# Performance work log

Measured on AMD Instinct MI355X. Metric: run time of the kernel, lower is better.

The kernel has to match this reference:

```python
import jax, jax.numpy as jnp
import numpy as np

D_MODEL = 1024
NUM_HEADS = 16
HEAD_DIM = D_MODEL // NUM_HEADS


def setup_inputs() -> dict:
    key = jax.random.key(0)
    k1, k2, k3, k4, k5 = jax.random.split(key, 5)
    B, S, D = 2, 2048, D_MODEL
    x = jax.random.normal(k1, (B, S, D), dtype=jnp.float32)
    mask = jnp.zeros((S, S), dtype=jnp.float32)  # additive mask, broadcast over [H,B,S,S]
    # torch nn.Linear params: weight [out, in], bias [out]
    scale_qkv = 1.0 / np.sqrt(D)
    W_qkv = jax.random.uniform(k2, (3 * D, D), jnp.float32, -scale_qkv, scale_qkv)
    b_qkv = jax.random.uniform(k3, (3 * D,), jnp.float32, -scale_qkv, scale_qkv)
    W_out = jax.random.uniform(k4, (D, D), jnp.float32, -scale_qkv, scale_qkv)
    b_out = jax.random.uniform(k5, (D,), jnp.float32, -scale_qkv, scale_qkv)
    return {"x": x, "mask": mask, "W_qkv": W_qkv, "b_qkv": b_qkv, "W_out": W_out, "b_out": b_out}


def reference(x, mask, W_qkv, b_qkv, W_out, b_out):
    B, S, D = x.shape
    H, hd = NUM_HEADS, HEAD_DIM
    # qkv projection: Linear(d, 3d) -> reshape [B,S,H,3*hd] -> [B,H,S,3*hd] -> chunk
    qkv = jnp.einsum('bsd,ed->bse', x, W_qkv) + b_qkv          # [B,S,3D]
    qkv = qkv.reshape(B, S, H, 3 * hd).transpose(0, 2, 1, 3)   # [B,H,S,3*hd]
    q, k, v = jnp.split(qkv, 3, axis=-1)                       # each [B,H,S,hd]
    scaled = jnp.einsum('bhqd,bhkd->bhqk', q, k) / jnp.sqrt(jnp.float32(hd))
    scaled = scaled + mask                                      # [S,S] broadcasts like the permuted add
    attn = jax.nn.softmax(scaled, axis=-1)
    values = jnp.einsum('bhqk,bhkd->bhqd', attn, v)            # [B,H,S,hd]
    values = values.transpose(0, 2, 1, 3).reshape(B, S, H * hd)
    out = jnp.einsum('bsd,ed->bse', values, W_out) + b_out
    return out
```

## Files before the change

### kernel.cpp

```cpp
#include <hip/hip_runtime.h>

#define SEQ   2048
#define BATCH 2
#define NH    16
#define HD    64
#define DM    1024

typedef unsigned short u16;
typedef unsigned int   u32;
typedef __attribute__((ext_vector_type(8))) short bf8;
typedef __attribute__((ext_vector_type(4))) float f4;

__device__ inline u16 f2bf(float f) {
    u32 u = __builtin_bit_cast(u32, f);
    return (u16)((u + 0x7FFFu + ((u >> 16) & 1u)) >> 16);
}

__device__ inline f4 MFMA(bf8 a, bf8 b, f4 c) {
    return __builtin_amdgcn_mfma_f32_16x16x32_bf16(a, b, c, 0, 0, 0);
}

__device__ inline void gload16(const u16* g, u16* l) {
    __builtin_amdgcn_global_load_lds(
        (const __attribute__((address_space(1))) unsigned int*)(const void*)g,
        (__attribute__((address_space(3))) unsigned int*)(void*)l, 16, 0, 0);
}

#define N4_X  1048576
#define N4_WQ 786432
#define N4_WO 262144
__global__ __launch_bounds__(256) void cast_all(const float* __restrict__ x,
                                                const float* __restrict__ wq,
                                                const float* __restrict__ wo,
                                                u16* __restrict__ xb,
                                                u16* __restrict__ wqb,
                                                u16* __restrict__ wob) {
    const int i = blockIdx.x * 256 + threadIdx.x;
    const float* src;
    u16* dst;
    int j;
    if (i < N4_X)                { src = x;  dst = xb;  j = i; }
    else if (i < N4_X + N4_WQ)   { src = wq; dst = wqb; j = i - N4_X; }
    else                         { src = wo; dst = wob; j = i - N4_X - N4_WQ; }
    const float4 v = ((const float4*)src)[j];
    ushort4 o;
    o.x = f2bf(v.x); o.y = f2bf(v.y); o.z = f2bf(v.z); o.w = f2bf(v.w);
    ((ushort4*)dst)[j] = o;
}

template<int MODE>
__global__ __launch_bounds__(256) void gemm_bf16(const u16* __restrict__ A,
                                                 const u16* __restrict__ Bm,
                                                 const float* __restrict__ bias,
                                                 u16* __restrict__ q_o,
                                                 u16* __restrict__ k_o,
                                                 u16* __restrict__ v_o,
                                                 float* __restrict__ f_o) {
    __shared__ __align__(16) u16 Al[128 * 32];
    __shared__ __align__(16) u16 Bl[128 * 32];
    const int t  = threadIdx.x;
    const int l  = t & 63, w = t >> 6;
    const int n0 = blockIdx.x * 128, m0 = blockIdx.y * 128;
    const int wr = w >> 1, wc = w & 1;
    const int lr16 = l & 15, lg = l >> 4;

    const f4 zf = {0.f, 0.f, 0.f, 0.f};
    f4 acc[4][4];
#pragma unroll
    for (int m = 0; m < 4; ++m)
#pragma unroll
        for (int n = 0; n < 4; ++n) acc[m][n] = zf;

    const int rw = t >> 2;
    const int kc = t & 3;

    for (int k0 = 0; k0 < DM; k0 += 32) {
        __syncthreads();
        gload16(&A[(size_t)(m0 + rw) * DM + k0 + kc * 8],       &Al[rw * 32 + kc * 8]);
        gload16(&A[(size_t)(m0 + 64 + rw) * DM + k0 + kc * 8],  &Al[(64 + rw) * 32 + kc * 8]);
        gload16(&Bm[(size_t)(n0 + rw) * DM + k0 + kc * 8],      &Bl[rw * 32 + kc * 8]);
        gload16(&Bm[(size_t)(n0 + 64 + rw) * DM + k0 + kc * 8], &Bl[(64 + rw) * 32 + kc * 8]);
        __syncthreads();
        bf8 af[4], bfr[4];
#pragma unroll
        for (int m = 0; m < 4; ++m)
            af[m] = *(const bf8*)&Al[(wr * 64 + m * 16 + lr16) * 32 + lg * 8];
#pragma unroll
        for (int n = 0; n < 4; ++n)
            bfr[n] = *(const bf8*)&Bl[(wc * 64 + n * 16 + lr16) * 32 + lg * 8];
        __builtin_amdgcn_s_setprio(1);
#pragma unroll
        for (int m = 0; m < 4; ++m)
#pragma unroll
            for (int n = 0; n < 4; ++n)
                acc[m][n] = MFMA(af[m], bfr[n], acc[m][n]);
        __builtin_amdgcn_s_setprio(0);
    }

#pragma unroll
    for (int m = 0; m < 4; ++m)
#pragma unroll
        for (int n = 0; n < 4; ++n)
#pragma unroll
            for (int r = 0; r < 4; ++r) {
                const int M = m0 + wr * 64 + m * 16 + lg * 4 + r;
                const int N = n0 + wc * 64 + n * 16 + lr16;
                const float val = acc[m][n][r] + bias[N];
                if (MODE == 0) {
                    const int b = M >> 11, s = M & (SEQ - 1);
                    const int h = N / 192, f = N % 192;
                    const int seg = f >> 6, c = f & 63;
                    u16* dst = (seg == 0) ? q_o : ((seg == 1) ? k_o : v_o);
                    dst[(((size_t)(b * NH + h)) * SEQ + s) * HD + c] = f2bf(val);
                } else {
                    f_o[(size_t)M * DM + N] = val;
                }
            }
}

__global__ __launch_bounds__(256) void v_transpose(const u16* __restrict__ v,
                                                   u16* __restrict__ vt) {
    __shared__ u16 tl[64][65];
    const int t  = threadIdx.x;
    const int s0 = blockIdx.x * 64;
    const int bh = blockIdx.y;
    const u16* src = v + ((size_t)bh * SEQ + s0) * HD;
#pragma unroll
    for (int i = 0; i < 2; ++i) {
        const int c = i * 256 + t, s = c >> 3, cc = c & 7;
        const float4 d = *(const float4*)&src[s * HD + cc * 8];
        const u16* dp = (const u16*)&d;
#pragma unroll
        for (int j = 0; j < 8; ++j) tl[s][cc * 8 + j] = dp[j];
    }
    __syncthreads();
    u16* dst = vt + (size_t)bh * HD * SEQ + s0;
#pragma unroll
    for (int i = 0; i < 2; ++i) {
        const int c = i * 256 + t, dim = c >> 3, sc = c & 7;
        __align__(16) u16 tmp[8];
#pragma unroll
        for (int j = 0; j < 8; ++j) tmp[j] = tl[sc * 8 + j][dim];
        *(float4*)&dst[(size_t)dim * SEQ + sc * 8] = *(const float4*)tmp;
    }
}

#define KS 72
__global__ __launch_bounds__(256) void flash_attn(const u16* __restrict__ qg,
                                                  const u16* __restrict__ kg,
                                                  const u16* __restrict__ vtg,
                                                  const float* __restrict__ mask,
                                                  u16* __restrict__ og) {
    __shared__ __align__(16) u16 Kl[2][64 * KS];
    __shared__ __align__(16) u16 Vl[2][64 * KS];
    __shared__ __align__(16) u16 Pl[4 * 16 * KS];
    const int t = threadIdx.x, l = t & 63, w = t >> 6;
    const int lr16 = l & 15, lg = l >> 4;
    const int q0 = blockIdx.x * 64;
    const int h = blockIdx.y, b = blockIdx.z;
    const int bh = b * NH + h;
    const int qbase = q0 + w * 16;

    bf8 qf[2];
    {
        const u16* qp = qg + ((size_t)bh * SEQ + qbase + lr16) * HD + lg * 8;
        qf[0] = *(const bf8*)qp;
        qf[1] = *(const bf8*)(qp + 32);
    }

    const f4 zf = {0.f, 0.f, 0.f, 0.f};
    f4 Oa[4];
    float mr[4], lrow[4];
#pragma unroll
    for (int n = 0; n < 4; ++n) Oa[n] = zf;
#pragma unroll
    for (int r = 0; r < 4; ++r) { mr[r] = -1e30f; lrow[r] = 0.f; }

    const u16* Kb = kg + (size_t)bh * SEQ * HD;
    const u16* Vb = vtg + (size_t)bh * HD * SEQ;
    u16* Pw = &Pl[w * 16 * KS];

    float4 kvr[2], vvr[2];
    float mk[4][4], mkn[4][4];

    auto issue_kv = [&](int kv0) {
#pragma unroll
        for (int i = 0; i < 2; ++i) {
            const int c = i * 256 + t, a = c >> 3, cc = c & 7;
            kvr[i] = *(const float4*)&Kb[(size_t)(kv0 + a) * HD + cc * 8];
            vvr[i] = *(const float4*)&Vb[(size_t)a * SEQ + kv0 + cc * 8];
        }
    };
    auto write_kv = [&](int buf) {
#pragma unroll
        for (int i = 0; i < 2; ++i) {
            const int c = i * 256 + t, a = c >> 3, cc = c & 7;
            *(float4*)&Kl[buf][a * KS + cc * 8] = kvr[i];
            *(float4*)&Vl[buf][a * KS + cc * 8] = vvr[i];
        }
    };
    auto issue_mask = [&](float (&m)[4][4], int kv0) {
#pragma unroll
        for (int n = 0; n < 4; ++n)
#pragma unroll
            for (int r = 0; r < 4; ++r)
                m[n][r] = mask[(size_t)(q0 + w * 16 + lg * 4 + r) * SEQ + kv0 + n * 16 + lr16];
    };

    issue_kv(0);
    issue_mask(mk, 0);
    write_kv(0);
    issue_kv(64);
    issue_mask(mkn, 64);
    __syncthreads();

    for (int kt = 0; kt < 32; ++kt) {
        const int cur = kt & 1;
        f4 sc[4];
        __builtin_amdgcn_s_setprio(1);
#pragma unroll
        for (int n = 0; n < 4; ++n) {
            const bf8 k0 = *(const bf8*)&Kl[cur][(n * 16 + lr16) * KS + lg * 8];
            const bf8 k1 = *(const bf8*)&Kl[cur][(n * 16 + lr16) * KS + 32 + lg * 8];
            f4 s = zf;
            s = MFMA(qf[0], k0, s);
            s = MFMA(qf[1], k1, s);
            sc[n] = s;
        }
        __builtin_amdgcn_s_setprio(0);
#pragma unroll
        for (int n = 0; n < 4; ++n)
#pragma unroll
            for (int r = 0; r < 4; ++r)
                sc[n][r] = sc[n][r] * 0.125f + mk[n][r];
        float pmax[4];
#pragma unroll
        for (int r = 0; r < 4; ++r) {
            float mx = fmaxf(fmaxf(sc[0][r], sc[1][r]), fmaxf(sc[2][r], sc[3][r]));
#pragma unroll
            for (int d = 1; d < 16; d <<= 1) mx = fmaxf(mx, __shfl_xor(mx, d));
            pmax[r] = mx;
        }
        bool need = false;
#pragma unroll
        for (int r = 0; r < 4; ++r) need |= (pmax[r] > mr[r] + 8.f);
        if (__any(need)) {
#pragma unroll
            for (int r = 0; r < 4; ++r) {
                const float mn = fmaxf(mr[r], pmax[r]);
                const float al = __expf(mr[r] - mn);
                mr[r] = mn;
                lrow[r] *= al;
#pragma unroll
                for (int n = 0; n < 4; ++n) Oa[n][r] *= al;
            }
        }
        float rs[4] = {0.f, 0.f, 0.f, 0.f};
        u16 pb[4][4];
#pragma unroll
        for (int n = 0; n < 4; ++n)
#pragma unroll
            for (int r = 0; r < 4; ++r) {
                const float p = __expf(sc[n][r] - mr[r]);
                rs[r] += p;
                pb[n][r] = f2bf(p);
            }
#pragma unroll
        for (int r = 0; r < 4; ++r) {
            float s = rs[r];
#pragma unroll
            for (int d = 1; d < 16; d <<= 1) s += __shfl_xor(s, d);
            lrow[r] += s;
        }
#pragma unroll
        for (int n = 0; n < 4; ++n)
#pragma unroll
            for (int r = 0; r < 4; ++r)
                Pw[(lg * 4 + r) * KS + n * 16 + lr16] = pb[n][r];
        asm volatile("s_waitcnt lgkmcnt(0)" ::: "memory");
        const bf8 pf0 = *(const bf8*)&Pw[lr16 * KS + lg * 8];
        const bf8 pf1 = *(const bf8*)&Pw[lr16 * KS + 32 + lg * 8];
        __builtin_amdgcn_s_setprio(1);
#pragma unroll
        for (int n = 0; n < 4; ++n) {
            const bf8 v0 = *(const bf8*)&Vl[cur][(n * 16 + lr16) * KS + lg * 8];
            const bf8 v1 = *(const bf8*)&Vl[cur][(n * 16 + lr16) * KS + 32 + lg * 8];
            Oa[n] = MFMA(pf0, v0, Oa[n]);
            Oa[n] = MFMA(pf1, v1, Oa[n]);
        }
        __builtin_amdgcn_s_setprio(0);
        if (kt < 31) {
            write_kv(cur ^ 1);
#pragma unroll
            for (int n = 0; n < 4; ++n)
#pragma unroll
                for (int r = 0; r < 4; ++r) mk[n][r] = mkn[n][r];
            if (kt < 30) {
                issue_kv((kt + 2) * 64);
                issue_mask(mkn, (kt + 2) * 64);
            }
        }
        __syncthreads();
    }

    float inv[4];
#pragma unroll
    for (int r = 0; r < 4; ++r) inv[r] = 1.f / lrow[r];
    __syncthreads();
    u16* Ol = Pl;
#pragma unroll
    for (int n = 0; n < 4; ++n)
#pragma unroll
        for (int r = 0; r < 4; ++r)
            Ol[(w * 16 + lg * 4 + r) * KS + n * 16 + lr16] = f2bf(Oa[n][r] * inv[r]);
    __syncthreads();
    {
        const int row = t >> 2, c0 = (t & 3) * 16;
        const u16* src = &Ol[row * KS + c0];
        u16* dstp = og + ((size_t)(b * SEQ + q0 + row)) * DM + h * HD + c0;
        const float4 o0 = *(const float4*)src;
        const float4 o1 = *(const float4*)(src + 8);
        *(float4*)dstp = o0;
        *(float4*)(dstp + 8) = o1;
    }
}

extern "C" void kernel_launch(void* const* d_in, const int* in_sizes, int n_in,
                              void* d_out, int out_size, void* d_ws, size_t ws_size,
                              hipStream_t stream) {
    const float* x     = (const float*)d_in[0];
    const float* mask  = (const float*)d_in[1];
    const float* W_qkv = (const float*)d_in[2];
    const float* b_qkv = (const float*)d_in[3];
    const float* W_out = (const float*)d_in[4];
    const float* b_out = (const float*)d_in[5];
    float* out = (float*)d_out;

    const size_t NQ = (size_t)BATCH * NH * SEQ * HD;
    u16* ws  = (u16*)d_ws;
    u16* xb  = ws;
    u16* wqb = xb + (size_t)4096 * 1024;
    u16* wob = wqb + (size_t)3072 * 1024;
    u16* qb  = wob + (size_t)1024 * 1024;
    u16* kb  = qb + NQ;
    u16* vb  = kb + NQ;
    u16* vtb = vb + NQ;
    u16* ob  = vtb + NQ;

    cast_all<<<(N4_X + N4_WQ + N4_WO) / 256, 256, 0, stream>>>(x, W_qkv, W_out, xb, wqb, wob);
    gemm_bf16<0><<<dim3(24, 32), 256, 0, stream>>>(xb, wqb, b_qkv, qb, kb, vb, nullptr);
    v_transpose<<<dim3(32, 32), 256, 0, stream>>>(vb, vtb);
    flash_attn<<<dim3(SEQ / 64, NH, BATCH), 256, 0, stream>>>(qb, kb, vtb, mask, ob);
    gemm_bf16<1><<<dim3(8, 32), 256, 0, stream>>>(ob, wob, b_out, nullptr, nullptr, nullptr, out);
}
```

Baseline: 346.3 us.

## Process 32 query rows per wave in flash attention with exp2 softmax

```diff
diff --git a/kernel.cpp b/kernel.cpp
--- a/kernel.cpp
+++ b/kernel.cpp
@@ -1,4 +1,5 @@
 #include <hip/hip_runtime.h>
+#include <hip/hip_bf16.h>
 
 #define SEQ   2048
 #define BATCH 2
@@ -146,6 +147,7 @@
 }
 
 #define KS 72
+#define QW 32
 __global__ __launch_bounds__(256) void flash_attn(const u16* __restrict__ qg,
                                                   const u16* __restrict__ kg,
                                                   const u16* __restrict__ vtg,
@@ -153,35 +155,44 @@
                                                   u16* __restrict__ og) {
     __shared__ __align__(16) u16 Kl[2][64 * KS];
     __shared__ __align__(16) u16 Vl[2][64 * KS];
-    __shared__ __align__(16) u16 Pl[4 * 16 * KS];
+    __shared__ __align__(16) u16 Pl[4 * QW * KS];
     const int t = threadIdx.x, l = t & 63, w = t >> 6;
     const int lr16 = l & 15, lg = l >> 4;
-    const int q0 = blockIdx.x * 64;
-    const int h = blockIdx.y, b = blockIdx.z;
-    const int bh = b * NH + h;
-    const int qbase = q0 + w * 16;
-
-    bf8 qf[2];
-    {
-        const u16* qp = qg + ((size_t)bh * SEQ + qbase + lr16) * HD + lg * 8;
-        qf[0] = *(const bf8*)qp;
-        qf[1] = *(const bf8*)(qp + 32);
+    const int bx = blockIdx.x;
+    const int qt = bx >> 5, bh = bx & 31;
+    const int h = bh & 15, b = bh >> 4;
+    const int q0 = qt * 128;
+    const int qbase = q0 + w * QW;
+
+    const float C1 = 0.18033688011f;
+    const float L2E = 1.44269504089f;
+
+    bf8 qf[2][2];
+#pragma unroll
+    for (int m = 0; m < 2; ++m) {
+        const u16* qp = qg + ((size_t)bh * SEQ + qbase + m * 16 + lr16) * HD + lg * 8;
+        qf[m][0] = *(const bf8*)qp;
+        qf[m][1] = *(const bf8*)(qp + 32);
     }
 
     const f4 zf = {0.f, 0.f, 0.f, 0.f};
-    f4 Oa[4];
-    float mr[4], lrow[4];
-#pragma unroll
-    for (int n = 0; n < 4; ++n) Oa[n] = zf;
-#pragma unroll
-    for (int r = 0; r < 4; ++r) { mr[r] = -1e30f; lrow[r] = 0.f; }
+    f4 Oa[2][4];
+    float mr2[2][4], lp[2][4];
+#pragma unroll
+    for (int m = 0; m < 2; ++m)
+#pragma unroll
+        for (int n = 0; n < 4; ++n) Oa[m][n] = zf;
+#pragma unroll
+    for (int m = 0; m < 2; ++m)
+#pragma unroll
+        for (int r = 0; r < 4; ++r) { mr2[m][r] = -1e30f; lp[m][r] = 0.f; }
 
     const u16* Kb = kg + (size_t)bh * SEQ * HD;
     const u16* Vb = vtg + (size_t)bh * HD * SEQ;
-    u16* Pw = &Pl[w * 16 * KS];
+    u16* Pw = &Pl[w * QW * KS];
 
     float4 kvr[2], vvr[2];
-    float mk[4][4], mkn[4][4];
+    float mk2[2][4][4], mkn2[2][4][4];
 
     auto issue_kv = [&](int kv0) {
 #pragma unroll
@@ -199,129 +210,147 @@
             *(float4*)&Vl[buf][a * KS + cc * 8] = vvr[i];
         }
     };
-    auto issue_mask = [&](float (&m)[4][4], int kv0) {
-#pragma unroll
-        for (int n = 0; n < 4; ++n)
-#pragma unroll
-            for (int r = 0; r < 4; ++r)
-                m[n][r] = mask[(size_t)(q0 + w * 16 + lg * 4 + r) * SEQ + kv0 + n * 16 + lr16];
+    auto issue_mask = [&](float (&mm)[2][4][4], int kv0) {
+#pragma unroll
+        for (int m = 0; m < 2; ++m)
+#pragma unroll
+            for (int n = 0; n < 4; ++n)
+#pragma unroll
+                for (int r = 0; r < 4; ++r)
+                    mm[m][n][r] = mask[(size_t)(qbase + m * 16 + lg * 4 + r) * SEQ
+                                       + kv0 + n * 16 + lr16] * L2E;
     };
 
     issue_kv(0);
-    issue_mask(mk, 0);
+    issue_mask(mk2, 0);
     write_kv(0);
     issue_kv(64);
-    issue_mask(mkn, 64);
+    issue_mask(mkn2, 64);
     __syncthreads();
 
     for (int kt = 0; kt < 32; ++kt) {
         const int cur = kt & 1;
-        f4 sc[4];
+        f4 sc[2][4];
         __builtin_amdgcn_s_setprio(1);
 #pragma unroll
         for (int n = 0; n < 4; ++n) {
             const bf8 k0 = *(const bf8*)&Kl[cur][(n * 16 + lr16) * KS + lg * 8];
             const bf8 k1 = *(const bf8*)&Kl[cur][(n * 16 + lr16) * KS + 32 + lg * 8];
-            f4 s = zf;
-            s = MFMA(qf[0], k0, s);
-            s = MFMA(qf[1], k1, s);
-            sc[n] = s;
+#pragma unroll
+            for (int m = 0; m < 2; ++m)
+                sc[m][n] = MFMA(qf[m][1], k1, MFMA(qf[m][0], k0, zf));
         }
         __builtin_amdgcn_s_setprio(0);
 #pragma unroll
-        for (int n = 0; n < 4; ++n)
-#pragma unroll
-            for (int r = 0; r < 4; ++r)
-                sc[n][r] = sc[n][r] * 0.125f + mk[n][r];
-        float pmax[4];
-#pragma unroll
-        for (int r = 0; r < 4; ++r) {
-            float mx = fmaxf(fmaxf(sc[0][r], sc[1][r]), fmaxf(sc[2][r], sc[3][r]));
-#pragma unroll
-            for (int d = 1; d < 16; d <<= 1) mx = fmaxf(mx, __shfl_xor(mx, d));
-            pmax[r] = mx;
-        }
+        for (int m = 0; m < 2; ++m)
+#pragma unroll
+            for (int n = 0; n < 4; ++n)
+#pragma unroll
+                for (int r = 0; r < 4; ++r)
+                    sc[m][n][r] = fmaf(sc[m][n][r], C1, mk2[m][n][r]);
+        float lmax[2][4];
         bool need = false;
 #pragma unroll
-        for (int r = 0; r < 4; ++r) need |= (pmax[r] > mr[r] + 8.f);
+        for (int m = 0; m < 2; ++m)
+#pragma unroll
+            for (int r = 0; r < 4; ++r) {
+                lmax[m][r] = fmaxf(fmaxf(sc[m][0][r], sc[m][1][r]),
+                                   fmaxf(sc[m][2][r], sc[m][3][r]));
+                need |= (lmax[m][r] > mr2[m][r] + 8.f);
+            }
         if (__any(need)) {
 #pragma unroll
+            for (int m = 0; m < 2; ++m)
+#pragma unroll
+                for (int r = 0; r < 4; ++r) {
+                    float mx = lmax[m][r];
+#pragma unroll
+                    for (int d = 1; d < 16; d <<= 1) mx = fmaxf(mx, __shfl_xor(mx, d));
+                    const float mn = fmaxf(mr2[m][r], mx);
+                    const float al = exp2f(mr2[m][r] - mn);
+                    mr2[m][r] = mn;
+                    lp[m][r] *= al;
+#pragma unroll
+                    for (int n = 0; n < 4; ++n) Oa[m][n][r] *= al;
+                }
+        }
+#pragma unroll
+        for (int m = 0; m < 2; ++m)
+#pragma unroll
             for (int r = 0; r < 4; ++r) {
-                const float mn = fmaxf(mr[r], pmax[r]);
-                const float al = __expf(mr[r] - mn);
-                mr[r] = mn;
-                lrow[r] *= al;
-#pragma unroll
-                for (int n = 0; n < 4; ++n) Oa[n][r] *= al;
-            }
-        }
-        float rs[4] = {0.f, 0.f, 0.f, 0.f};
-        u16 pb[4][4];
-#pragma unroll
-        for (int n = 0; n < 4; ++n)
-#pragma unroll
-            for (int r = 0; r < 4; ++r) {
-                const float p = __expf(sc[n][r] - mr[r]);
-                rs[r] += p;
-                pb[n][r] = f2bf(p);
-            }
-#pragma unroll
-        for (int r = 0; r < 4; ++r) {
-            float s = rs[r];
-#pragma unroll
-            for (int d = 1; d < 16; d <<= 1) s += __shfl_xor(s, d);
-            lrow[r] += s;
-        }
-#pragma unroll
-        for (int n = 0; n < 4; ++n)
-#pragma unroll
-            for (int r = 0; r < 4; ++r)
-                Pw[(lg * 4 + r) * KS + n * 16 + lr16] = pb[n][r];
+                float ps = 0.f;
+#pragma unroll
+                for (int n = 0; n < 4; ++n) {
+                    const float p = exp2f(sc[m][n][r] - mr2[m][r]);
+                    ps += p;
+                    const __hip_bfloat16 hb = __float2bfloat16(p);
+                    Pw[(m * 16 + lg * 4 + r) * KS + n * 16 + lr16] =
+                        __builtin_bit_cast(u16, hb);
+                }
+                lp[m][r] += ps;
+            }
         asm volatile("s_waitcnt lgkmcnt(0)" ::: "memory");
-        const bf8 pf0 = *(const bf8*)&Pw[lr16 * KS + lg * 8];
-        const bf8 pf1 = *(const bf8*)&Pw[lr16 * KS + 32 + lg * 8];
+        bf8 pf[2][2];
+#pragma unroll
+        for (int m = 0; m < 2; ++m) {
+            pf[m][0] = *(const bf8*)&Pw[(m * 16 + lr16) * KS + lg * 8];
+            pf[m][1] = *(const bf8*)&Pw[(m * 16 + lr16) * KS + 32 + lg * 8];
+        }
         __builtin_amdgcn_s_setprio(1);
 #pragma unroll
         for (int n = 0; n < 4; ++n) {
             const bf8 v0 = *(const bf8*)&Vl[cur][(n * 16 + lr16) * KS + lg * 8];
             const bf8 v1 = *(const bf8*)&Vl[cur][(n * 16 + lr16) * KS + 32 + lg * 8];
-            Oa[n] = MFMA(pf0, v0, Oa[n]);
-            Oa[n] = MFMA(pf1, v1, Oa[n]);
+#pragma unroll
+            for (int m = 0; m < 2; ++m) {
+                Oa[m][n] = MFMA(pf[m][0], v0, Oa[m][n]);
+                Oa[m][n] = MFMA(pf[m][1], v1, Oa[m][n]);
+            }
         }
         __builtin_amdgcn_s_setprio(0);
         if (kt < 31) {
             write_kv(cur ^ 1);
 #pragma unroll
-            for (int n = 0; n < 4; ++n)
-#pragma unroll
-                for (int r = 0; r < 4; ++r) mk[n][r] = mkn[n][r];
+            for (int m = 0; m < 2; ++m)
+#pragma unroll
+                for (int n = 0; n < 4; ++n)
+#pragma unroll
+                    for (int r = 0; r < 4; ++r) mk2[m][n][r] = mkn2[m][n][r];
             if (kt < 30) {
                 issue_kv((kt + 2) * 64);
-                issue_mask(mkn, (kt + 2) * 64);
+                issue_mask(mkn2, (kt + 2) * 64);
             }
         }
         __syncthreads();
     }
 
-    float inv[4];
-#pragma unroll
-    for (int r = 0; r < 4; ++r) inv[r] = 1.f / lrow[r];
-    __syncthreads();
+    float inv[2][4];
+#pragma unroll
+    for (int m = 0; m < 2; ++m)
+#pragma unroll
+        for (int r = 0; r < 4; ++r) {
+            float s = lp[m][r];
+#pragma unroll
+            for (int d = 1; d < 16; d <<= 1) s += __shfl_xor(s, d);
+            inv[m][r] = 1.f / s;
+        }
     u16* Ol = Pl;
 #pragma unroll
-    for (int n = 0; n < 4; ++n)
-#pragma unroll
-        for (int r = 0; r < 4; ++r)
-            Ol[(w * 16 + lg * 4 + r) * KS + n * 16 + lr16] = f2bf(Oa[n][r] * inv[r]);
+    for (int m = 0; m < 2; ++m)
+#pragma unroll
+        for (int n = 0; n < 4; ++n)
+#pragma unroll
+            for (int r = 0; r < 4; ++r)
+                Ol[(w * QW + m * 16 + lg * 4 + r) * KS + n * 16 + lr16] =
+                    f2bf(Oa[m][n][r] * inv[m][r]);
     __syncthreads();
     {
-        const int row = t >> 2, c0 = (t & 3) * 16;
+        const int row = t >> 1, c0 = (t & 1) * 32;
         const u16* src = &Ol[row * KS + c0];
         u16* dstp = og + ((size_t)(b * SEQ + q0 + row)) * DM + h * HD + c0;
-        const float4 o0 = *(const float4*)src;
-        const float4 o1 = *(const float4*)(src + 8);
-        *(float4*)dstp = o0;
-        *(float4*)(dstp + 8) = o1;
+#pragma unroll
+        for (int j = 0; j < 4; ++j)
+            *(float4*)(dstp + j * 8) = *(const float4*)(src + j * 8);
     }
 }
 
@@ -350,6 +379,6 @@
     cast_all<<<(N4_X + N4_WQ + N4_WO) / 256, 256, 0, stream>>>(x, W_qkv, W_out, xb, wqb, wob);
     gemm_bf16<0><<<dim3(24, 32), 256, 0, stream>>>(xb, wqb, b_qkv, qb, kb, vb, nullptr);
     v_transpose<<<dim3(32, 32), 256, 0, stream>>>(vb, vtb);
-    flash_attn<<<dim3(SEQ / 64, NH, BATCH), 256, 0, stream>>>(qb, kb, vtb, mask, ob);
+    flash_attn<<<dim3((SEQ / 128) * NH * BATCH), 256, 0, stream>>>(qb, kb, vtb, mask, ob);
     gemm_bf16<1><<<dim3(8, 32), 256, 0, stream>>>(ob, wob, b_out, nullptr, nullptr, nullptr, out);
 }
```

Result: slower. 367.2 us (+6.1%).

## Restructure flash attention into single-wave blocks loading K/V directly into registers

Applied to the files above, without the earlier changes.

```diff
diff --git a/kernel.cpp b/kernel.cpp
--- a/kernel.cpp
+++ b/kernel.cpp
@@ -1,4 +1,5 @@
 #include <hip/hip_runtime.h>
+#include <hip/hip_bf16.h>
 
 #define SEQ   2048
 #define BATCH 2
@@ -146,20 +147,21 @@
 }
 
 #define KS 72
-__global__ __launch_bounds__(256) void flash_attn(const u16* __restrict__ qg,
-                                                  const u16* __restrict__ kg,
-                                                  const u16* __restrict__ vtg,
-                                                  const float* __restrict__ mask,
-                                                  u16* __restrict__ og) {
-    __shared__ __align__(16) u16 Kl[2][64 * KS];
-    __shared__ __align__(16) u16 Vl[2][64 * KS];
-    __shared__ __align__(16) u16 Pl[4 * 16 * KS];
-    const int t = threadIdx.x, l = t & 63, w = t >> 6;
+__global__ __launch_bounds__(64, 3) void flash_attn(const u16* __restrict__ qg,
+                                                    const u16* __restrict__ kg,
+                                                    const u16* __restrict__ vtg,
+                                                    const float* __restrict__ mask,
+                                                    u16* __restrict__ og) {
+    __shared__ __align__(16) u16 Pw[16 * KS];
+    const int l = threadIdx.x;
     const int lr16 = l & 15, lg = l >> 4;
-    const int q0 = blockIdx.x * 64;
-    const int h = blockIdx.y, b = blockIdx.z;
-    const int bh = b * NH + h;
-    const int qbase = q0 + w * 16;
+    const int bx = blockIdx.x;
+    const int qt = bx >> 5, bh = bx & 31;
+    const int h = bh & 15, b = bh >> 4;
+    const int qbase = qt * 16;
+
+    const float C1  = 0.18033688011f;
+    const float L2E = 1.44269504089f;
 
     bf8 qf[2];
     {
@@ -170,158 +172,111 @@
 
     const f4 zf = {0.f, 0.f, 0.f, 0.f};
     f4 Oa[4];
-    float mr[4], lrow[4];
+    float mr[4], lp[4];
 #pragma unroll
     for (int n = 0; n < 4; ++n) Oa[n] = zf;
 #pragma unroll
-    for (int r = 0; r < 4; ++r) { mr[r] = -1e30f; lrow[r] = 0.f; }
-
-    const u16* Kb = kg + (size_t)bh * SEQ * HD;
-    const u16* Vb = vtg + (size_t)bh * HD * SEQ;
-    u16* Pw = &Pl[w * 16 * KS];
-
-    float4 kvr[2], vvr[2];
-    float mk[4][4], mkn[4][4];
-
-    auto issue_kv = [&](int kv0) {
-#pragma unroll
-        for (int i = 0; i < 2; ++i) {
-            const int c = i * 256 + t, a = c >> 3, cc = c & 7;
-            kvr[i] = *(const float4*)&Kb[(size_t)(kv0 + a) * HD + cc * 8];
-            vvr[i] = *(const float4*)&Vb[(size_t)a * SEQ + kv0 + cc * 8];
-        }
-    };
-    auto write_kv = [&](int buf) {
-#pragma unroll
-        for (int i = 0; i < 2; ++i) {
-            const int c = i * 256 + t, a = c >> 3, cc = c & 7;
-            *(float4*)&Kl[buf][a * KS + cc * 8] = kvr[i];
-            *(float4*)&Vl[buf][a * KS + cc * 8] = vvr[i];
-        }
-    };
-    auto issue_mask = [&](float (&m)[4][4], int kv0) {
+    for (int r = 0; r < 4; ++r) { mr[r] = -1e30f; lp[r] = 0.f; }
+
+    const u16* Kb  = kg  + (size_t)bh * SEQ * HD;
+    const u16* Vtb = vtg + (size_t)bh * HD * SEQ;
+    const float* Mrow = mask + (size_t)(qbase + lg * 4) * SEQ;
+
+    for (int kt = 0; kt < 32; ++kt) {
+        const int kv0 = kt * 64;
+        float mk[4][4];
 #pragma unroll
         for (int n = 0; n < 4; ++n)
 #pragma unroll
             for (int r = 0; r < 4; ++r)
-                m[n][r] = mask[(size_t)(q0 + w * 16 + lg * 4 + r) * SEQ + kv0 + n * 16 + lr16];
-    };
-
-    issue_kv(0);
-    issue_mask(mk, 0);
-    write_kv(0);
-    issue_kv(64);
-    issue_mask(mkn, 64);
-    __syncthreads();
-
-    for (int kt = 0; kt < 32; ++kt) {
-        const int cur = kt & 1;
+                mk[n][r] = Mrow[(size_t)r * SEQ + kv0 + n * 16 + lr16] * L2E;
+        bf8 kf[4][2], vf[4][2];
+#pragma unroll
+        for (int n = 0; n < 4; ++n) {
+            const u16* kp = &Kb[(size_t)(kv0 + n * 16 + lr16) * HD + lg * 8];
+            kf[n][0] = *(const bf8*)kp;
+            kf[n][1] = *(const bf8*)(kp + 32);
+            const u16* vp = &Vtb[(size_t)(n * 16 + lr16) * SEQ + kv0 + lg * 8];
+            vf[n][0] = *(const bf8*)vp;
+            vf[n][1] = *(const bf8*)(vp + 32);
+        }
         f4 sc[4];
         __builtin_amdgcn_s_setprio(1);
 #pragma unroll
-        for (int n = 0; n < 4; ++n) {
-            const bf8 k0 = *(const bf8*)&Kl[cur][(n * 16 + lr16) * KS + lg * 8];
-            const bf8 k1 = *(const bf8*)&Kl[cur][(n * 16 + lr16) * KS + 32 + lg * 8];
-            f4 s = zf;
-            s = MFMA(qf[0], k0, s);
-            s = MFMA(qf[1], k1, s);
-            sc[n] = s;
-        }
+        for (int n = 0; n < 4; ++n)
+            sc[n] = MFMA(qf[1], kf[n][1], MFMA(qf[0], kf[n][0], zf));
         __builtin_amdgcn_s_setprio(0);
 #pragma unroll
         for (int n = 0; n < 4; ++n)
 #pragma unroll
             for (int r = 0; r < 4; ++r)
-                sc[n][r] = sc[n][r] * 0.125f + mk[n][r];
-        float pmax[4];
+                sc[n][r] = fmaf(sc[n][r], C1, mk[n][r]);
+        float lmax[4];
+        bool need = false;
 #pragma unroll
         for (int r = 0; r < 4; ++r) {
-            float mx = fmaxf(fmaxf(sc[0][r], sc[1][r]), fmaxf(sc[2][r], sc[3][r]));
-#pragma unroll
-            for (int d = 1; d < 16; d <<= 1) mx = fmaxf(mx, __shfl_xor(mx, d));
-            pmax[r] = mx;
-        }
-        bool need = false;
-#pragma unroll
-        for (int r = 0; r < 4; ++r) need |= (pmax[r] > mr[r] + 8.f);
+            lmax[r] = fmaxf(fmaxf(sc[0][r], sc[1][r]), fmaxf(sc[2][r], sc[3][r]));
+            need |= (lmax[r] > mr[r] + 8.f);
+        }
         if (__any(need)) {
 #pragma unroll
             for (int r = 0; r < 4; ++r) {
-                const float mn = fmaxf(mr[r], pmax[r]);
-                const float al = __expf(mr[r] - mn);
+                float mx = lmax[r];
+#pragma unroll
+                for (int d = 1; d < 16; d <<= 1) mx = fmaxf(mx, __shfl_xor(mx, d));
+                const float mn = fmaxf(mr[r], mx);
+                const float al = exp2f(mr[r] - mn);
                 mr[r] = mn;
-                lrow[r] *= al;
+                lp[r] *= al;
 #pragma unroll
                 for (int n = 0; n < 4; ++n) Oa[n][r] *= al;
             }
         }
-        float rs[4] = {0.f, 0.f, 0.f, 0.f};
-        u16 pb[4][4];
-#pragma unroll
-        for (int n = 0; n < 4; ++n)
-#pragma unroll
-            for (int r = 0; r < 4; ++r) {
-                const float p = __expf(sc[n][r] - mr[r]);
-                rs[r] += p;
-                pb[n][r] = f2bf(p);
+#pragma unroll
+        for (int r = 0; r < 4; ++r) {
+            float ps = 0.f;
+#pragma unroll
+            for (int n = 0; n < 4; ++n) {
+                const float p = exp2f(sc[n][r] - mr[r]);
+                ps += p;
+                const __hip_bfloat16 hb = __float2bfloat16(p);
+                Pw[(lg * 4 + r) * KS + n * 16 + lr16] = __builtin_bit_cast(u16, hb);
             }
-#pragma unroll
-        for (int r = 0; r < 4; ++r) {
-            float s = rs[r];
-#pragma unroll
-            for (int d = 1; d < 16; d <<= 1) s += __shfl_xor(s, d);
-            lrow[r] += s;
-        }
-#pragma unroll
-        for (int n = 0; n < 4; ++n)
-#pragma unroll
-            for (int r = 0; r < 4; ++r)
-                Pw[(lg * 4 + r) * KS + n * 16 + lr16] = pb[n][r];
+            lp[r] += ps;
+        }
         asm volatile("s_waitcnt lgkmcnt(0)" ::: "memory");
         const bf8 pf0 = *(const bf8*)&Pw[lr16 * KS + lg * 8];
         const bf8 pf1 = *(const bf8*)&Pw[lr16 * KS + 32 + lg * 8];
         __builtin_amdgcn_s_setprio(1);
 #pragma unroll
         for (int n = 0; n < 4; ++n) {
-            const bf8 v0 = *(const bf8*)&Vl[cur][(n * 16 + lr16) * KS + lg * 8];
-            const bf8 v1 = *(const bf8*)&Vl[cur][(n * 16 + lr16) * KS + 32 + lg * 8];
-            Oa[n] = MFMA(pf0, v0, Oa[n]);
-            Oa[n] = MFMA(pf1, v1, Oa[n]);
+            Oa[n] = MFMA(pf0, vf[n][0], Oa[n]);
+            Oa[n] = MFMA(pf1, vf[n][1], Oa[n]);
         }
         __builtin_amdgcn_s_setprio(0);
-        if (kt < 31) {
-            write_kv(cur ^ 1);
-#pragma unroll
-            for (int n = 0; n < 4; ++n)
-#pragma unroll
-                for (int r = 0; r < 4; ++r) mk[n][r] = mkn[n][r];
-            if (kt < 30) {
-                issue_kv((kt + 2) * 64);
-                issue_mask(mkn, (kt + 2) * 64);
-            }
-        }
-        __syncthreads();
     }
 
     float inv[4];
 #pragma unroll
-    for (int r = 0; r < 4; ++r) inv[r] = 1.f / lrow[r];
-    __syncthreads();
-    u16* Ol = Pl;
+    for (int r = 0; r < 4; ++r) {
+        float s = lp[r];
+#pragma unroll
+        for (int d = 1; d < 16; d <<= 1) s += __shfl_xor(s, d);
+        inv[r] = 1.f / s;
+    }
+    u16* Ol = Pw;
 #pragma unroll
     for (int n = 0; n < 4; ++n)
 #pragma unroll
         for (int r = 0; r < 4; ++r)
-            Ol[(w * 16 + lg * 4 + r) * KS + n * 16 + lr16] = f2bf(Oa[n][r] * inv[r]);
-    __syncthreads();
+            Ol[(lg * 4 + r) * KS + n * 16 + lr16] = f2bf(Oa[n][r] * inv[r]);
+    asm volatile("s_waitcnt lgkmcnt(0)" ::: "memory");
     {
-        const int row = t >> 2, c0 = (t & 3) * 16;
+        const int row = l >> 2, c0 = (l & 3) * 16;
         const u16* src = &Ol[row * KS + c0];
-        u16* dstp = og + ((size_t)(b * SEQ + q0 + row)) * DM + h * HD + c0;
-        const float4 o0 = *(const float4*)src;
-        const float4 o1 = *(const float4*)(src + 8);
-        *(float4*)dstp = o0;
-        *(float4*)(dstp + 8) = o1;
+        u16* dstp = og + ((size_t)(b * SEQ + qbase + row)) * DM + h * HD + c0;
+        *(float4*)dstp       = *(const float4*)src;
+        *(float4*)(dstp + 8) = *(const float4*)(src + 8);
     }
 }
 
@@ -350,6 +305,6 @@
     cast_all<<<(N4_X + N4_WQ + N4_WO) / 256, 256, 0, stream>>>(x, W_qkv, W_out, xb, wqb, wob);
     gemm_bf16<0><<<dim3(24, 32), 256, 0, stream>>>(xb, wqb, b_qkv, qb, kb, vb, nullptr);
     v_transpose<<<dim3(32, 32), 256, 0, stream>>>(vb, vtb);
-    flash_attn<<<dim3(SEQ / 64, NH, BATCH), 256, 0, stream>>>(qb, kb, vtb, mask, ob);
+    flash_attn<<<dim3((SEQ / 16) * NH * BATCH), 64, 0, stream>>>(qb, kb, vtb, mask, ob);
     gemm_bf16<1><<<dim3(8, 32), 256, 0, stream>>>(ob, wob, b_out, nullptr, nullptr, nullptr, out);
 }
```

Result: slower. 414.0 us (+19.6%).

## Compute transposed S tile in flash attention and pass P through shuffles instead of LDS

Applied to the files above, without the earlier changes.

```diff
diff --git a/kernel.cpp b/kernel.cpp
--- a/kernel.cpp
+++ b/kernel.cpp
@@ -1,4 +1,5 @@
 #include <hip/hip_runtime.h>
+#include <hip/hip_bf16.h>
 
 #define SEQ   2048
 #define BATCH 2
@@ -10,6 +11,7 @@
 typedef unsigned int   u32;
 typedef __attribute__((ext_vector_type(8))) short bf8;
 typedef __attribute__((ext_vector_type(4))) float f4;
+typedef __attribute__((ext_vector_type(4))) u32  u32x4;
 
 __device__ inline u16 f2bf(float f) {
     u32 u = __builtin_bit_cast(u32, f);
@@ -146,20 +148,24 @@
 }
 
 #define KS 72
-__global__ __launch_bounds__(256) void flash_attn(const u16* __restrict__ qg,
-                                                  const u16* __restrict__ kg,
-                                                  const u16* __restrict__ vtg,
-                                                  const float* __restrict__ mask,
-                                                  u16* __restrict__ og) {
+__global__ __launch_bounds__(256, 4) void flash_attn(const u16* __restrict__ qg,
+                                                     const u16* __restrict__ kg,
+                                                     const u16* __restrict__ vtg,
+                                                     const float* __restrict__ mask,
+                                                     u16* __restrict__ og) {
     __shared__ __align__(16) u16 Kl[2][64 * KS];
     __shared__ __align__(16) u16 Vl[2][64 * KS];
-    __shared__ __align__(16) u16 Pl[4 * 16 * KS];
     const int t = threadIdx.x, l = t & 63, w = t >> 6;
     const int lr16 = l & 15, lg = l >> 4;
-    const int q0 = blockIdx.x * 64;
-    const int h = blockIdx.y, b = blockIdx.z;
-    const int bh = b * NH + h;
+    const int bid = blockIdx.x;
+    const int lb  = (bid & 7) * 128 + (bid >> 3);
+    const int bh  = lb >> 5, qt = lb & 31;
+    const int h = bh & 15, b = bh >> 4;
+    const int q0 = qt * 64;
     const int qbase = q0 + w * 16;
+
+    const float C1  = 0.18033688011f;
+    const float L2E = 1.44269504089f;
 
     bf8 qf[2];
     {
@@ -170,18 +176,15 @@
 
     const f4 zf = {0.f, 0.f, 0.f, 0.f};
     f4 Oa[4];
-    float mr[4], lrow[4];
 #pragma unroll
     for (int n = 0; n < 4; ++n) Oa[n] = zf;
-#pragma unroll
-    for (int r = 0; r < 4; ++r) { mr[r] = -1e30f; lrow[r] = 0.f; }
-
-    const u16* Kb = kg + (size_t)bh * SEQ * HD;
+    float mr = -1e30f, lp = 0.f;
+
+    const u16* Kb = kg  + (size_t)bh * SEQ * HD;
     const u16* Vb = vtg + (size_t)bh * HD * SEQ;
-    u16* Pw = &Pl[w * 16 * KS];
 
     float4 kvr[2], vvr[2];
-    float mk[4][4], mkn[4][4];
+    f4 mk[4], mkn[4];
 
     auto issue_kv = [&](int kv0) {
 #pragma unroll
@@ -199,12 +202,15 @@
             *(float4*)&Vl[buf][a * KS + cc * 8] = vvr[i];
         }
     };
-    auto issue_mask = [&](float (&m)[4][4], int kv0) {
-#pragma unroll
-        for (int n = 0; n < 4; ++n)
-#pragma unroll
-            for (int r = 0; r < 4; ++r)
-                m[n][r] = mask[(size_t)(q0 + w * 16 + lg * 4 + r) * SEQ + kv0 + n * 16 + lr16];
+    auto issue_mask = [&](f4 (&mm)[4], int kv0) {
+        const float* mrow = &mask[(size_t)(qbase + lr16) * SEQ + kv0 + lg * 4];
+#pragma unroll
+        for (int kb = 0; kb < 4; ++kb) {
+            f4 v = *(const f4*)(mrow + kb * 16);
+#pragma unroll
+            for (int r = 0; r < 4; ++r) v[r] *= L2E;
+            mm[kb] = v;
+        }
     };
 
     issue_kv(0);
@@ -219,82 +225,81 @@
         f4 sc[4];
         __builtin_amdgcn_s_setprio(1);
 #pragma unroll
-        for (int n = 0; n < 4; ++n) {
-            const bf8 k0 = *(const bf8*)&Kl[cur][(n * 16 + lr16) * KS + lg * 8];
-            const bf8 k1 = *(const bf8*)&Kl[cur][(n * 16 + lr16) * KS + 32 + lg * 8];
-            f4 s = zf;
-            s = MFMA(qf[0], k0, s);
-            s = MFMA(qf[1], k1, s);
-            sc[n] = s;
+        for (int kb = 0; kb < 4; ++kb) {
+            const bf8 k0 = *(const bf8*)&Kl[cur][(kb * 16 + lr16) * KS + lg * 8];
+            const bf8 k1 = *(const bf8*)&Kl[cur][(kb * 16 + lr16) * KS + 32 + lg * 8];
+            sc[kb] = MFMA(k1, qf[1], MFMA(k0, qf[0], zf));
         }
         __builtin_amdgcn_s_setprio(0);
 #pragma unroll
-        for (int n = 0; n < 4; ++n)
+        for (int kb = 0; kb < 4; ++kb)
 #pragma unroll
             for (int r = 0; r < 4; ++r)
-                sc[n][r] = sc[n][r] * 0.125f + mk[n][r];
-        float pmax[4];
-#pragma unroll
-        for (int r = 0; r < 4; ++r) {
-            float mx = fmaxf(fmaxf(sc[0][r], sc[1][r]), fmaxf(sc[2][r], sc[3][r]));
-#pragma unroll
-            for (int d = 1; d < 16; d <<= 1) mx = fmaxf(mx, __shfl_xor(mx, d));
-            pmax[r] = mx;
-        }
-        bool need = false;
-#pragma unroll
-        for (int r = 0; r < 4; ++r) need |= (pmax[r] > mr[r] + 8.f);
-        if (__any(need)) {
-#pragma unroll
-            for (int r = 0; r < 4; ++r) {
-                const float mn = fmaxf(mr[r], pmax[r]);
-                const float al = __expf(mr[r] - mn);
-                mr[r] = mn;
-                lrow[r] *= al;
-#pragma unroll
-                for (int n = 0; n < 4; ++n) Oa[n][r] *= al;
-            }
-        }
-        float rs[4] = {0.f, 0.f, 0.f, 0.f};
-        u16 pb[4][4];
-#pragma unroll
-        for (int n = 0; n < 4; ++n)
-#pragma unroll
-            for (int r = 0; r < 4; ++r) {
-                const float p = __expf(sc[n][r] - mr[r]);
-                rs[r] += p;
-                pb[n][r] = f2bf(p);
-            }
-#pragma unroll
-        for (int r = 0; r < 4; ++r) {
-            float s = rs[r];
-#pragma unroll
-            for (int d = 1; d < 16; d <<= 1) s += __shfl_xor(s, d);
-            lrow[r] += s;
-        }
-#pragma unroll
-        for (int n = 0; n < 4; ++n)
-#pragma unroll
-            for (int r = 0; r < 4; ++r)
-                Pw[(lg * 4 + r) * KS + n * 16 + lr16] = pb[n][r];
-        asm volatile("s_waitcnt lgkmcnt(0)" ::: "memory");
-        const bf8 pf0 = *(const bf8*)&Pw[lr16 * KS + lg * 8];
-        const bf8 pf1 = *(const bf8*)&Pw[lr16 * KS + 32 + lg * 8];
+                sc[kb][r] = fmaf(sc[kb][r], C1, mk[kb][r]);
+        float rmax = fmaxf(
+            fmaxf(fmaxf(fmaxf(sc[0][0], sc[0][1]), fmaxf(sc[0][2], sc[0][3])),
+                  fmaxf(fmaxf(sc[1][0], sc[1][1]), fmaxf(sc[1][2], sc[1][3]))),
+            fmaxf(fmaxf(fmaxf(sc[2][0], sc[2][1]), fmaxf(sc[2][2], sc[2][3])),
+                  fmaxf(fmaxf(sc[3][0], sc[3][1]), fmaxf(sc[3][2], sc[3][3]))));
+        rmax = fmaxf(rmax, __shfl_xor(rmax, 16));
+        rmax = fmaxf(rmax, __shfl_xor(rmax, 32));
+        if (__any(rmax > mr + 8.f)) {
+            const float mn = fmaxf(mr, rmax);
+            const float al = exp2f(mr - mn);
+            mr = mn;
+            lp *= al;
+            float alr[4];
+#pragma unroll
+            for (int r = 0; r < 4; ++r) alr[r] = __shfl(al, lg * 4 + r);
+#pragma unroll
+            for (int n = 0; n < 4; ++n)
+#pragma unroll
+                for (int r = 0; r < 4; ++r) Oa[n][r] *= alr[r];
+        }
+        u32 pk[4][2];
+#pragma unroll
+        for (int kb = 0; kb < 4; ++kb) {
+            const float p0 = exp2f(sc[kb][0] - mr);
+            const float p1 = exp2f(sc[kb][1] - mr);
+            const float p2 = exp2f(sc[kb][2] - mr);
+            const float p3 = exp2f(sc[kb][3] - mr);
+            lp += (p0 + p1) + (p2 + p3);
+            pk[kb][0] = ((u32)f2bf(p1) << 16) | f2bf(p0);
+            pk[kb][1] = ((u32)f2bf(p3) << 16) | f2bf(p2);
+        }
+        const int s0 = (lg & 1) * 32 + lr16, s1 = s0 + 16;
+        const bool hi = (lg & 2) != 0;
+        u32x4 paw[2];
+#pragma unroll
+        for (int hf = 0; hf < 2; ++hf) {
+            const int kbA = hf * 2, kbB = hf * 2 + 1;
+            const u32 a0 = (u32)__shfl((int)pk[kbA][0], s0);
+            const u32 a1 = (u32)__shfl((int)pk[kbA][1], s0);
+            const u32 a2 = (u32)__shfl((int)pk[kbA][0], s1);
+            const u32 a3 = (u32)__shfl((int)pk[kbA][1], s1);
+            const u32 b0 = (u32)__shfl((int)pk[kbB][0], s0);
+            const u32 b1 = (u32)__shfl((int)pk[kbB][1], s0);
+            const u32 b2 = (u32)__shfl((int)pk[kbB][0], s1);
+            const u32 b3 = (u32)__shfl((int)pk[kbB][1], s1);
+            paw[hf][0] = hi ? b0 : a0;
+            paw[hf][1] = hi ? b1 : a1;
+            paw[hf][2] = hi ? b2 : a2;
+            paw[hf][3] = hi ? b3 : a3;
+        }
+        const bf8 pa0 = __builtin_bit_cast(bf8, paw[0]);
+        const bf8 pa1 = __builtin_bit_cast(bf8, paw[1]);
         __builtin_amdgcn_s_setprio(1);
 #pragma unroll
         for (int n = 0; n < 4; ++n) {
             const bf8 v0 = *(const bf8*)&Vl[cur][(n * 16 + lr16) * KS + lg * 8];
             const bf8 v1 = *(const bf8*)&Vl[cur][(n * 16 + lr16) * KS + 32 + lg * 8];
-            Oa[n] = MFMA(pf0, v0, Oa[n]);
-            Oa[n] = MFMA(pf1, v1, Oa[n]);
+            Oa[n] = MFMA(pa1, v1, MFMA(pa0, v0, Oa[n]));
         }
         __builtin_amdgcn_s_setprio(0);
         if (kt < 31) {
             write_kv(cur ^ 1);
 #pragma unroll
-            for (int n = 0; n < 4; ++n)
-#pragma unroll
-                for (int r = 0; r < 4; ++r) mk[n][r] = mkn[n][r];
+            for (int kb = 0; kb < 4; ++kb) mk[kb] = mkn[kb];
             if (kt < 30) {
                 issue_kv((kt + 2) * 64);
                 issue_mask(mkn, (kt + 2) * 64);
@@ -303,25 +308,25 @@
         __syncthreads();
     }
 
-    float inv[4];
-#pragma unroll
-    for (int r = 0; r < 4; ++r) inv[r] = 1.f / lrow[r];
-    __syncthreads();
-    u16* Ol = Pl;
+    lp += __shfl_xor(lp, 16);
+    lp += __shfl_xor(lp, 32);
+    const float inv = 1.f / lp;
+    float invr[4];
+#pragma unroll
+    for (int r = 0; r < 4; ++r) invr[r] = __shfl(inv, lg * 4 + r);
+    u16* Ol = &Kl[0][0];
 #pragma unroll
     for (int n = 0; n < 4; ++n)
 #pragma unroll
         for (int r = 0; r < 4; ++r)
-            Ol[(w * 16 + lg * 4 + r) * KS + n * 16 + lr16] = f2bf(Oa[n][r] * inv[r]);
+            Ol[(w * 16 + lg * 4 + r) * KS + n * 16 + lr16] = f2bf(Oa[n][r] * invr[r]);
     __syncthreads();
     {
         const int row = t >> 2, c0 = (t & 3) * 16;
         const u16* src = &Ol[row * KS + c0];
         u16* dstp = og + ((size_t)(b * SEQ + q0 + row)) * DM + h * HD + c0;
-        const float4 o0 = *(const float4*)src;
-        const float4 o1 = *(const float4*)(src + 8);
-        *(float4*)dstp = o0;
-        *(float4*)(dstp + 8) = o1;
+        *(float4*)dstp       = *(const float4*)src;
+        *(float4*)(dstp + 8) = *(const float4*)(src + 8);
     }
 }
 
@@ -350,6 +355,6 @@
     cast_all<<<(N4_X + N4_WQ + N4_WO) / 256, 256, 0, stream>>>(x, W_qkv, W_out, xb, wqb, wob);
     gemm_bf16<0><<<dim3(24, 32), 256, 0, stream>>>(xb, wqb, b_qkv, qb, kb, vb, nullptr);
     v_transpose<<<dim3(32, 32), 256, 0, stream>>>(vb, vtb);
-    flash_attn<<<dim3(SEQ / 64, NH, BATCH), 256, 0, stream>>>(qb, kb, vtb, mask, ob);
+    flash_attn<<<dim3(32 * NH * BATCH), 256, 0, stream>>>(qb, kb, vtb, mask, ob);
     gemm_bf16<1><<<dim3(8, 32), 256, 0, stream>>>(ob, wob, b_out, nullptr, nullptr, nullptr, out);
 }
```

Result: slower. 410.3 us (+18.5%).
